# Optimization experiments

Hardware: AMD Instinct MI355X
Metric: run time of the kernel (lower is better)

## Reference

```python
import jax, jax.numpy as jnp
import numpy as np

THETA0 = 3.0
THETA = 5.0


def _edt(bg):
    """Exact Euclidean distance transform.
    bg: [B,H,W] bool, True where distance is 0 (the 'background'/feature set).
    Returns [B,H,W] float32 distance of every pixel to the nearest True pixel.
    Separable two-pass algorithm: 1D pass along H via scan, then exact
    min over column offsets along W (Meijster lower-envelope done densely).
    """
    B, H, W = bg.shape
    big = jnp.float32(H + W)
    f = bg.astype(jnp.float32)
    xs = jnp.moveaxis(f, 1, 0)  # [H,B,W] scan over rows

    def step(carry, row):
        d = jnp.where(row > 0, 0.0, carry + 1.0)
        return d, d

    init = jnp.full((B, W), big, jnp.float32)
    _, gf = jax.lax.scan(step, init, xs)                  # top-down
    _, gb = jax.lax.scan(step, init, xs, reverse=True)    # bottom-up
    g = jnp.minimum(gf, gb)            # [H,B,W] 1D vertical distance
    g = jnp.moveaxis(g, 0, 1)          # [B,H,W]
    g2 = jnp.minimum(g, big) ** 2
    col = jnp.arange(W, dtype=jnp.float32)
    off2 = (col[:, None] - col[None, :]) ** 2             # [j,k]
    # d2[b,i,j] = min_k g2[b,i,k] + (j-k)^2   -> [B,H,W,W] intermediate
    d2 = jnp.min(g2[:, :, None, :] + off2[None, None, :, :], axis=-1)
    return jnp.sqrt(d2)


def reference(predictions, targets):
    # predictions: [B,1,H,W] logits; targets: [B,1,H,W] binary masks
    t = targets[:, 0]                                   # [B,H,W]
    fg = t > 0.5
    dist_pos = _edt(~fg)   # distance_transform_edt(target): dist to nearest 0
    dist_neg = _edt(fg)    # distance_transform_edt(1-target): dist to nearest 1
    dist_map = jnp.where(fg, dist_pos, -dist_neg)
    # weight = 1 / (1 + exp((|d| - theta0)/theta)) == sigmoid(-(|d|-theta0)/theta)
    weight = jax.nn.sigmoid(-(jnp.abs(dist_map) - THETA0) / THETA)[:, None]  # [B,1,H,W]
    # numerically stable BCE-with-logits == BCE(sigmoid(x), t)
    x = predictions
    bce = jnp.maximum(x, 0.0) - x * targets + jnp.log1p(jnp.exp(-jnp.abs(x)))
    return jnp.mean(bce * weight)


def setup_inputs() -> dict:
    key = jax.random.key(0)
    k1, k2 = jax.random.split(key)
    B, C, H, W = 8, 1, 256, 256
    predictions = jax.random.normal(k1, (B, C, H, W), dtype=jnp.float32)
    targets = jax.random.randint(k2, (B, C, H, W), 0, 2).astype(jnp.float32)
    return {"predictions": predictions, "targets": targets}
```

## Files before the change

kernel.cpp:

```cpp
#include <hip/hip_runtime.h>
#include <math.h>

#define BB 8
#define HH 256
#define WW 256
#define NPIX (BB*HH*WW)
#define BIGI 512
#define BIGBIG (1<<20)

#define P_OFF   (2 * NPIX)
#define P_STRIDE 32
#define C_OFF   (P_OFF + 16 * P_STRIDE)

__global__ __launch_bounds__(512) void edt_vertical_bits(
    const float* __restrict__ tgt,
    float* __restrict__ ws) {
  __shared__ unsigned int smem[8 * 64];

  if (blockIdx.x == 0) {
    if (threadIdx.x < 16) ws[P_OFF + threadIdx.x * P_STRIDE] = 0.0f;
    if (threadIdx.x == 16) ((int*)ws)[C_OFF] = 0;
  }

  float* gA2 = ws;
  float* gB2 = ws + NPIX;

  int k = threadIdx.x >> 6;
  int l = threadIdx.x & 63;
  int b = blockIdx.x >> 2;
  int w0 = (blockIdx.x & 3) << 6;
  size_t ibase = (size_t)b * (HH * WW) + (size_t)w0 + l;

  unsigned int m = 0;
#pragma unroll
  for (int i = 0; i < 32; ++i) {
    float t = tgt[ibase + (size_t)(32 * k + i) * WW];
    m |= (t > 0.5f ? 1u : 0u) << i;
  }
  smem[k * 64 + l] = m;
  __syncthreads();

  unsigned int Mf[8];
#pragma unroll
  for (int j = 0; j < 8; ++j) Mf[j] = smem[j * 64 + l];

  int fcA = BIGBIG, fcB = BIGBIG;
  {
    int cA = BIGBIG, cB = BIGBIG;
#pragma unroll
    for (int j = 0; j < 8; ++j) {
      if (j == k) { fcA = cA; fcB = cB; }
      unsigned int a = ~Mf[j], bm = Mf[j];
      cA = a  ? (int)__builtin_clz(a)  : cA + 32;
      cB = bm ? (int)__builtin_clz(bm) : cB + 32;
    }
  }
  int bcA = BIGBIG, bcB = BIGBIG;
  {
    int cA = BIGBIG, cB = BIGBIG;
#pragma unroll
    for (int j = 7; j >= 0; --j) {
      if (j == k) { bcA = cA; bcB = cB; }
      unsigned int a = ~Mf[j], bm = Mf[j];
      cA = a  ? (int)__builtin_ctz(a)  : cA + 32;
      cB = bm ? (int)__builtin_ctz(bm) : cB + 32;
    }
  }

  unsigned int mB = m;
  unsigned int mA = ~m;
  size_t obase = ibase + (size_t)(32 * k) * WW;

#pragma unroll 8
  for (int rr = 0; rr < 32; ++rr) {
    {
      unsigned int x = mA << (31 - rr);
      unsigned int y = mA >> rr;
      int df = x ? (int)__builtin_clz(x) : (rr + 1 + fcA);
      int db = y ? (int)__builtin_ctz(y) : (32 - rr + bcA);
      int d = min(min(df, db), BIGI);
      gA2[obase + (size_t)rr * WW] = (float)(d * d);
    }
    {
      unsigned int x = mB << (31 - rr);
      unsigned int y = mB >> rr;
      int df = x ? (int)__builtin_clz(x) : (rr + 1 + fcB);
      int db = y ? (int)__builtin_ctz(y) : (32 - rr + bcB);
      int d = min(min(df, db), BIGI);
      gB2[obase + (size_t)rr * WW] = (float)(d * d);
    }
  }
}

#define ENV_GROUP(kk) { float4 v = s4[kk];                        \
    float D0 = fw - (float)(4 * (kk));                            \
    d2 = fminf(d2, fmaf(D0, D0, v.x));                            \
    float D1 = D0 - 1.0f; d2 = fminf(d2, fmaf(D1, D1, v.y));      \
    float D2 = D0 - 2.0f; d2 = fminf(d2, fmaf(D2, D2, v.z));      \
    float D3 = D0 - 3.0f; d2 = fminf(d2, fmaf(D3, D3, v.w)); }

__global__ __launch_bounds__(1024) void edt_row_loss3(
    const float* __restrict__ pred,
    const float* __restrict__ tgt,
    float* __restrict__ ws,
    float* __restrict__ out) {
  __shared__ __align__(16) float lA[4][WW];
  __shared__ __align__(16) float lB[4][WW];
  __shared__ float wsum[16];
  __shared__ int lastFlag;

  const float* gA2 = ws;
  const float* gB2 = ws + NPIX;
  float* partials = ws + P_OFF;
  int* counter = ((int*)ws) + C_OFF;

  int tid = threadIdx.x;
  size_t base = (size_t)blockIdx.x * (4 * WW);

  ((float*)lA)[tid] = gA2[base + tid];
  ((float*)lB)[tid] = gB2[base + tid];
  float x = pred[base + tid];
  float t = tgt[base + tid];
  __syncthreads();

  int r = tid >> 8;
  int w = tid & 255;
  bool fg = t > 0.5f;
  const float4* s4 = (const float4*)(fg ? lA[r] : lB[r]);

  int w0 = w & ~63;
  int kc0 = w0 >> 2;
  float fw = (float)w;
  float d2 = 1e30f;

#pragma unroll 4
  for (int k = kc0; k < kc0 + 16; ++k) ENV_GROUP(k);

  int kL = kc0 - 1;
  int kR = kc0 + 16;
  for (int iter = 0; iter < 16; ++iter) {
    int bL = (kL >= 0) ? (w0 - 4 * kL - 3) : 100000;
    int bR = (kR <= 63) ? (4 * kR - w0 - 63) : 100000;
    int bb = min(bL, bR);
    float bb2 = (float)bb * (float)bb;
    if (__all(d2 <= bb2)) break;
    if (kL >= 0) { ENV_GROUP(kL); kL--; }
    if (kR <= 63) { ENV_GROUP(kR); kR++; }
  }

  float dd = sqrtf(d2);
  float weight = 1.0f / (1.0f + __expf((dd - 3.0f) * 0.2f));
  float bce = fmaxf(x, 0.0f) - x * t + log1pf(__expf(-fabsf(x)));
  float c = bce * weight * (1.0f / (float)NPIX);

#pragma unroll
  for (int off = 32; off > 0; off >>= 1) c += __shfl_down(c, off, 64);
  if ((tid & 63) == 0) wsum[tid >> 6] = c;
  __syncthreads();

  if (tid < 64) {
    float v = (tid < 16) ? wsum[tid] : 0.0f;
#pragma unroll
    for (int off = 8; off > 0; off >>= 1) v += __shfl_down(v, off, 64);
    if (tid == 0) {
      atomicAdd(&partials[(blockIdx.x & 15) * P_STRIDE], v);
      __threadfence();
      int done = atomicAdd(counter, 1);
      lastFlag = (done == (int)gridDim.x - 1) ? 1 : 0;
    }
  }
  __syncthreads();

  if (lastFlag && tid < 64) {
    float v = (tid < 16) ? atomicAdd(&partials[tid * P_STRIDE], 0.0f) : 0.0f;
#pragma unroll
    for (int off = 8; off > 0; off >>= 1) v += __shfl_down(v, off, 64);
    if (tid == 0) out[0] = v;
  }
}

extern "C" void kernel_launch(void* const* d_in, const int* in_sizes, int n_in,
                              void* d_out, int out_size, void* d_ws, size_t ws_size,
                              hipStream_t stream) {
  const float* pred = (const float*)d_in[0];
  const float* tgt  = (const float*)d_in[1];
  float* out = (float*)d_out;
  float* ws  = (float*)d_ws;

  edt_vertical_bits<<<dim3(32), dim3(512), 0, stream>>>(tgt, ws);
  edt_row_loss3<<<dim3(512), dim3(1024), 0, stream>>>(pred, tgt, ws, out);
}
```

Measured before the change: 75.88 us.

## Pack target bitmasks and compute vertical distances inside the row kernel

The first kernel now only packs each column's target into 32-bit masks (64 blocks instead of 32). It no longer writes two full float squared-distance maps to global memory. The row kernel reads the 8 column masks per pixel, recomputes the vertical distances directly into shared memory, and derives the target from the mask instead of rereading it. This removes about 4 MB of global writes and reads of intermediate maps, at the cost of redundant clz/ctz work per pixel in the second kernel.

```diff
diff --git a/kernel.cpp b/kernel.cpp
--- a/kernel.cpp
+++ b/kernel.cpp
@@ -12,84 +12,28 @@
 #define P_STRIDE 32
 #define C_OFF   (P_OFF + 16 * P_STRIDE)
 
-__global__ __launch_bounds__(512) void edt_vertical_bits(
+__global__ __launch_bounds__(256) void pack_masks(
     const float* __restrict__ tgt,
     float* __restrict__ ws) {
-  __shared__ unsigned int smem[8 * 64];
-
   if (blockIdx.x == 0) {
     if (threadIdx.x < 16) ws[P_OFF + threadIdx.x * P_STRIDE] = 0.0f;
     if (threadIdx.x == 16) ((int*)ws)[C_OFF] = 0;
   }
 
-  float* gA2 = ws;
-  float* gB2 = ws + NPIX;
-
-  int k = threadIdx.x >> 6;
-  int l = threadIdx.x & 63;
-  int b = blockIdx.x >> 2;
-  int w0 = (blockIdx.x & 3) << 6;
-  size_t ibase = (size_t)b * (HH * WW) + (size_t)w0 + l;
+  unsigned int* maskws = (unsigned int*)ws;
+  int j = threadIdx.x >> 5;
+  int c = threadIdx.x & 31;
+  int im = blockIdx.x >> 3;
+  int w = ((blockIdx.x & 7) << 5) + c;
+  size_t ibase = (size_t)im * (HH * WW) + w;
 
   unsigned int m = 0;
 #pragma unroll
   for (int i = 0; i < 32; ++i) {
-    float t = tgt[ibase + (size_t)(32 * k + i) * WW];
+    float t = tgt[ibase + (size_t)(32 * j + i) * WW];
     m |= (t > 0.5f ? 1u : 0u) << i;
   }
-  smem[k * 64 + l] = m;
-  __syncthreads();
-
-  unsigned int Mf[8];
-#pragma unroll
-  for (int j = 0; j < 8; ++j) Mf[j] = smem[j * 64 + l];
-
-  int fcA = BIGBIG, fcB = BIGBIG;
-  {
-    int cA = BIGBIG, cB = BIGBIG;
-#pragma unroll
-    for (int j = 0; j < 8; ++j) {
-      if (j == k) { fcA = cA; fcB = cB; }
-      unsigned int a = ~Mf[j], bm = Mf[j];
-      cA = a  ? (int)__builtin_clz(a)  : cA + 32;
-      cB = bm ? (int)__builtin_clz(bm) : cB + 32;
-    }
-  }
-  int bcA = BIGBIG, bcB = BIGBIG;
-  {
-    int cA = BIGBIG, cB = BIGBIG;
-#pragma unroll
-    for (int j = 7; j >= 0; --j) {
-      if (j == k) { bcA = cA; bcB = cB; }
-      unsigned int a = ~Mf[j], bm = Mf[j];
-      cA = a  ? (int)__builtin_ctz(a)  : cA + 32;
-      cB = bm ? (int)__builtin_ctz(bm) : cB + 32;
-    }
-  }
-
-  unsigned int mB = m;
-  unsigned int mA = ~m;
-  size_t obase = ibase + (size_t)(32 * k) * WW;
-
-#pragma unroll 8
-  for (int rr = 0; rr < 32; ++rr) {
-    {
-      unsigned int x = mA << (31 - rr);
-      unsigned int y = mA >> rr;
-      int df = x ? (int)__builtin_clz(x) : (rr + 1 + fcA);
-      int db = y ? (int)__builtin_ctz(y) : (32 - rr + bcA);
-      int d = min(min(df, db), BIGI);
-      gA2[obase + (size_t)rr * WW] = (float)(d * d);
-    }
-    {
-      unsigned int x = mB << (31 - rr);
-      unsigned int y = mB >> rr;
-      int df = x ? (int)__builtin_clz(x) : (rr + 1 + fcB);
-      int db = y ? (int)__builtin_ctz(y) : (32 - rr + bcB);
-      int d = min(min(df, db), BIGI);
-      gB2[obase + (size_t)rr * WW] = (float)(d * d);
-    }
-  }
+  maskws[im * 2048 + j * 256 + w] = m;
 }
 
 #define ENV_GROUP(kk) { float4 v = s4[kk];                        \
@@ -99,9 +43,8 @@
     float D2 = D0 - 2.0f; d2 = fminf(d2, fmaf(D2, D2, v.z));      \
     float D3 = D0 - 3.0f; d2 = fminf(d2, fmaf(D3, D3, v.w)); }
 
-__global__ __launch_bounds__(1024) void edt_row_loss3(
+__global__ __launch_bounds__(1024) void edt_row_loss4(
     const float* __restrict__ pred,
-    const float* __restrict__ tgt,
     float* __restrict__ ws,
     float* __restrict__ out) {
   __shared__ __align__(16) float lA[4][WW];
@@ -109,23 +52,71 @@
   __shared__ float wsum[16];
   __shared__ int lastFlag;
 
-  const float* gA2 = ws;
-  const float* gB2 = ws + NPIX;
+  const unsigned int* maskws = (const unsigned int*)ws;
   float* partials = ws + P_OFF;
   int* counter = ((int*)ws) + C_OFF;
 
   int tid = threadIdx.x;
-  size_t base = (size_t)blockIdx.x * (4 * WW);
+  int im = blockIdx.x >> 6;
+  int rg = blockIdx.x & 63;
+  int r = tid >> 8;
+  int w = tid & 255;
+  int R = 4 * rg + r;
+  int k = R >> 5;
+  int rr = R & 31;
 
-  ((float*)lA)[tid] = gA2[base + tid];
-  ((float*)lB)[tid] = gB2[base + tid];
-  float x = pred[base + tid];
-  float t = tgt[base + tid];
+  unsigned int M[8];
+#pragma unroll
+  for (int j = 0; j < 8; ++j) M[j] = maskws[im * 2048 + j * 256 + w];
+
+  float x = pred[(size_t)blockIdx.x * (4 * WW) + tid];
+
+  int fcA = BIGBIG, fcB = BIGBIG, bcA = BIGBIG, bcB = BIGBIG;
+  {
+    int cA = BIGBIG, cB = BIGBIG;
+#pragma unroll
+    for (int j = 0; j < 8; ++j) {
+      if (j == k) { fcA = cA; fcB = cB; }
+      unsigned int a = ~M[j], bm = M[j];
+      cA = a  ? (int)__builtin_clz(a)  : cA + 32;
+      cB = bm ? (int)__builtin_clz(bm) : cB + 32;
+    }
+  }
+  {
+    int cA = BIGBIG, cB = BIGBIG;
+#pragma unroll
+    for (int j = 7; j >= 0; --j) {
+      if (j == k) { bcA = cA; bcB = cB; }
+      unsigned int a = ~M[j], bm = M[j];
+      cA = a  ? (int)__builtin_ctz(a)  : cA + 32;
+      cB = bm ? (int)__builtin_ctz(bm) : cB + 32;
+    }
+  }
+
+  unsigned int mk = M[k];
+  bool fg = (mk >> rr) & 1u;
+  float t = fg ? 1.0f : 0.0f;
+
+  {
+    unsigned int mA = ~mk;
+    unsigned int xx = mA << (31 - rr);
+    unsigned int yy = mA >> rr;
+    int df = xx ? (int)__builtin_clz(xx) : (rr + 1 + fcA);
+    int db = yy ? (int)__builtin_ctz(yy) : (32 - rr + bcA);
+    int d = min(min(df, db), BIGI);
+    lA[r][w] = (float)(d * d);
+  }
+  {
+    unsigned int mB = mk;
+    unsigned int xx = mB << (31 - rr);
+    unsigned int yy = mB >> rr;
+    int df = xx ? (int)__builtin_clz(xx) : (rr + 1 + fcB);
+    int db = yy ? (int)__builtin_ctz(yy) : (32 - rr + bcB);
+    int d = min(min(df, db), BIGI);
+    lB[r][w] = (float)(d * d);
+  }
   __syncthreads();
 
-  int r = tid >> 8;
-  int w = tid & 255;
-  bool fg = t > 0.5f;
   const float4* s4 = (const float4*)(fg ? lA[r] : lB[r]);
 
   int w0 = w & ~63;
@@ -134,7 +125,7 @@
   float d2 = 1e30f;
 
 #pragma unroll 4
-  for (int k = kc0; k < kc0 + 16; ++k) ENV_GROUP(k);
+  for (int kk = kc0; kk < kc0 + 16; ++kk) ENV_GROUP(kk);
 
   int kL = kc0 - 1;
   int kR = kc0 + 16;
@@ -187,6 +178,6 @@
   float* out = (float*)d_out;
   float* ws  = (float*)d_ws;
 
-  edt_vertical_bits<<<dim3(32), dim3(512), 0, stream>>>(tgt, ws);
-  edt_row_loss3<<<dim3(512), dim3(1024), 0, stream>>>(pred, tgt, ws, out);
+  pack_masks<<<dim3(64), dim3(256), 0, stream>>>(tgt, ws);
+  edt_row_loss4<<<dim3(512), dim3(1024), 0, stream>>>(pred, ws, out);
 }
```

Measured after the change: 71.08 us. 1.07x faster.
